# Performance work log

Measured on AMD Instinct MI355X. Metric: run time of the kernel, lower is better.

Reference implementation:

```python
import jax, jax.numpy as jnp
import numpy as np
from jax import lax

B, S, T, E, H, V = 32, 64, 48, 512, 1024, 32000
PAD = 0


def lstm_cell(x, h, c, W_ih, W_hh, b_ih, b_hh):
    # PyTorch gate order: i, f, g, o
    gates = x @ W_ih.T + b_ih + h @ W_hh.T + b_hh
    i, f, g, o = jnp.split(gates, 4, axis=-1)
    c = jax.nn.sigmoid(f) * c + jax.nn.sigmoid(i) * jnp.tanh(g)
    h = jax.nn.sigmoid(o) * jnp.tanh(c)
    return h, c


def setup_inputs() -> dict:
    key = jax.random.key(0)
    ks = jax.random.split(key, 24)
    sc = 0.02
    n = lambda k, shape: jax.random.normal(k, shape, jnp.float32) * sc
    src_emb = n(ks[0], (V, E)).at[PAD].set(0.0)
    tgt_emb = n(ks[1], (V, E)).at[PAD].set(0.0)
    inp = {
        "input_sequences": jax.random.randint(ks[2], (B, S), 0, V),
        "target_sequences": jax.random.randint(ks[3], (B, T), 0, V),
        "src_emb": src_emb,
        "tgt_emb": tgt_emb,
        "enc_Wih_f": n(ks[4], (4 * H, E)),
        "enc_Whh_f": n(ks[5], (4 * H, H)),
        "enc_bih_f": n(ks[6], (4 * H,)),
        "enc_bhh_f": n(ks[7], (4 * H,)),
        "enc_Wih_b": n(ks[8], (4 * H, E)),
        "enc_Whh_b": n(ks[9], (4 * H, H)),
        "enc_bih_b": n(ks[10], (4 * H,)),
        "enc_bhh_b": n(ks[11], (4 * H,)),
        "dec_Wih": n(ks[12], (4 * H, E + H)),
        "dec_Whh": n(ks[13], (4 * H, H)),
        "dec_bih": n(ks[14], (4 * H,)),
        "dec_bhh": n(ks[15], (4 * H,)),
        "W_init_h": n(ks[16], (H, 2 * H)),
        "W_init_c": n(ks[17], (H, 2 * H)),
        "W_att": n(ks[18], (H, 2 * H)),
        "W_comb": n(ks[19], (H, 3 * H)),
        "W_proj": n(ks[20], (V, H)),
    }
    return inp


def reference(input_sequences, target_sequences, src_emb, tgt_emb,
              enc_Wih_f, enc_Whh_f, enc_bih_f, enc_bhh_f,
              enc_Wih_b, enc_Whh_b, enc_bih_b, enc_bhh_b,
              dec_Wih, dec_Whh, dec_bih, dec_bhh,
              W_init_h, W_init_c, W_att, W_comb, W_proj):
    bsz = input_sequences.shape[0]
    x_src = src_emb[input_sequences.T]  # (S, B, E) time-major

    def make_enc_step(W_ih, W_hh, b_ih, b_hh):
        def step(carry, x):
            h, c = carry
            h, c = lstm_cell(x, h, c, W_ih, W_hh, b_ih, b_hh)
            return (h, c), h
        return step

    h0 = jnp.zeros((bsz, H), x_src.dtype)
    c0 = jnp.zeros((bsz, H), x_src.dtype)
    # bidirectional encoder
    (hf, cf), hs_f = lax.scan(make_enc_step(enc_Wih_f, enc_Whh_f, enc_bih_f, enc_bhh_f), (h0, c0), x_src)
    (hb, cb), hs_b = lax.scan(make_enc_step(enc_Wih_b, enc_Whh_b, enc_bih_b, enc_bhh_b), (h0, c0), x_src[::-1])
    enc_h = jnp.concatenate([hs_f, hs_b[::-1]], axis=-1).transpose(1, 0, 2)  # (B, S, 2H)
    last_hidden = jnp.concatenate([hf, hb], axis=-1)  # (B, 2H)
    last_cell = jnp.concatenate([cf, cb], axis=-1)

    dec_h0 = last_hidden @ W_init_h.T
    dec_c0 = last_cell @ W_init_c.T
    enc_att = enc_h @ W_att.T  # (B, S, H)

    x_tgt = tgt_emb[target_sequences.T]  # (T, B, E)

    def dec_step(carry, e_t):
        h, c, prev_out = carry
        x = jnp.concatenate([e_t, prev_out], axis=-1)  # (B, E+H)
        h, c = lstm_cell(x, h, c, dec_Wih, dec_Whh, dec_bih, dec_bhh)
        scores = jnp.einsum('bh,bsh->bs', h, enc_att)
        attn = jax.nn.softmax(scores, axis=-1)
        ctx = jnp.einsum('bs,bsd->bd', attn, enc_h)  # (B, 2H)
        out = jnp.concatenate([h, ctx], axis=-1) @ W_comb.T  # (B, H)
        return (h, c, out), out

    prev0 = jnp.zeros((bsz, H), x_src.dtype)
    _, outs = lax.scan(dec_step, (dec_h0, dec_c0, prev0), x_tgt)  # (T, B, H)

    logits = outs @ W_proj.T  # (T, B, V)
    P = jax.nn.log_softmax(logits, axis=-1)
    tgt = target_sequences.T  # (T, B)
    # P[t] predicts tgt[t+1]; torch.gather with smaller index truncates P to T-1 steps
    gold = jnp.take_along_axis(P[:-1], tgt[1:][..., None], axis=-1)[..., 0]  # (T-1, B)
    scores = gold.sum(axis=0)  # (B,)
    return scores
```

## Files before the change

### kernel.cpp

```cpp
#include <hip/hip_runtime.h>

typedef short v8s __attribute__((ext_vector_type(8)));
typedef float v4f __attribute__((ext_vector_type(4)));
typedef unsigned short u16;

#define DI __device__ __forceinline__
#define MFMA(a, b, c) __builtin_amdgcn_mfma_f32_16x16x32_bf16(a, b, c, 0, 0, 0)

constexpr int B = 32, S = 64, T = 48, E = 512, H = 1024, V = 32000;
constexpr int TP = T - 1;
constexpr int MROWS = TP * B;
constexpr int NCH = 250;

DI u16 f2bf(float f) {
    unsigned u = __float_as_uint(f);
    unsigned r = (u + 0x7FFFu + ((u >> 16) & 1u)) >> 16;
    return (u16)r;
}
DI float bf2f(u16 h) { return __uint_as_float(((unsigned)h) << 16); }
DI v8s load8(const u16* p) { return *reinterpret_cast<const v8s*>(p); }

typedef __attribute__((address_space(1))) const unsigned int gu32;
typedef __attribute__((address_space(3))) unsigned int lu32;
DI void gload_lds16(const u16* g, u16* l) {
    __builtin_amdgcn_global_load_lds((gu32*)g, (lu32*)l, 16, 0, 0);
}

DI void cstore(unsigned* p, unsigned v) {
    __hip_atomic_store(p, v, __ATOMIC_RELAXED, __HIP_MEMORY_SCOPE_AGENT);
}
DI int cload(const int* p) {
    return __hip_atomic_load(p, __ATOMIC_RELAXED, __HIP_MEMORY_SCOPE_AGENT);
}

DI void gbar2(int* bar, int bid, int nblk, int v) {
    __syncthreads();
    if (bid == 0) {
        int t = threadIdx.x;
        if (t > 0 && t < nblk) {
            while (cload(bar + 16 + t * 4) < v) __builtin_amdgcn_s_sleep(1);
        }
        __syncthreads();
        if (t == 0)
            __hip_atomic_store(bar, v, __ATOMIC_RELAXED, __HIP_MEMORY_SCOPE_AGENT);
    } else {
        if (threadIdx.x == 0) {
            __hip_atomic_store(bar + 16 + bid * 4, v, __ATOMIC_RELAXED,
                               __HIP_MEMORY_SCOPE_AGENT);
            while (cload(bar) < v) __builtin_amdgcn_s_sleep(2);
        }
        __syncthreads();
    }
}

__global__ __launch_bounds__(256) void k_cvt(const float* __restrict__ s,
                                             u16* __restrict__ d, int n4) {
    int i = blockIdx.x * 256 + threadIdx.x;
    if (i >= n4) return;
    float4 v = reinterpret_cast<const float4*>(s)[i];
    ushort4 o;
    o.x = f2bf(v.x); o.y = f2bf(v.y); o.z = f2bf(v.z); o.w = f2bf(v.w);
    reinterpret_cast<ushort4*>(d)[i] = o;
}

struct CvtD {
    const float* src[11];
    u16* dst[11];
    int n4[11];
    int start[12];
};
__global__ __launch_bounds__(256) void k_cvtm(CvtD d) {
    int blk = blockIdx.x;
    int seg = 0;
    #pragma unroll
    for (int q = 0; q < 11; ++q)
        if (blk >= d.start[q + 1]) seg = q + 1;
    int i = (blk - d.start[seg]) * 256 + threadIdx.x;
    if (i >= d.n4[seg]) return;
    float4 v = reinterpret_cast<const float4*>(d.src[seg])[i];
    ushort4 o;
    o.x = f2bf(v.x); o.y = f2bf(v.y); o.z = f2bf(v.z); o.w = f2bf(v.w);
    reinterpret_cast<ushort4*>(d.dst[seg])[i] = o;
}

__global__ __launch_bounds__(256) void k_embed(const int* __restrict__ seq, int seqstr,
                                               int nsteps, const float* __restrict__ emb,
                                               u16* __restrict__ out) {
    int i = blockIdx.x * 256 + threadIdx.x;
    int total = nsteps * B * (E / 4);
    if (i >= total) return;
    int q = i & 127;
    int sb = i >> 7;
    int b = sb & 31;
    int s = sb >> 5;
    int tok = seq[b * seqstr + s];
    float4 v = reinterpret_cast<const float4*>(emb + (size_t)tok * E)[q];
    ushort4 o;
    o.x = f2bf(v.x); o.y = f2bf(v.y); o.z = f2bf(v.z); o.w = f2bf(v.w);
    reinterpret_cast<ushort4*>(out + ((size_t)(s * B + b)) * E)[q] = o;
}

__global__ __launch_bounds__(256) void k_ench(const u16* __restrict__ hsf,
                                              const u16* __restrict__ hsb,
                                              u16* __restrict__ ench) {
    int id = blockIdx.x * 256 + threadIdx.x;
    int d8 = id & 255; int s = (id >> 8) & 63; int b = id >> 14;
    int d0 = d8 * 8;
    const u16* src = (d0 < H) ? hsf + (((size_t)(s + 1) * B + b)) * H + d0
                              : hsb + (((size_t)(S - s) * B + b)) * H + (d0 - H);
    *reinterpret_cast<v8s*>(ench + ((size_t)b * S + s) * 2 * H + d0) = load8(src);
}

__global__ __launch_bounds__(256) void k_transp(const u16* __restrict__ in,
                                                u16* __restrict__ out, int K, int N) {
    __shared__ u16 t[64][72];
    int nt = blockIdx.x * 64, kt = blockIdx.y * 64;
    int tid = threadIdx.x;
    int r = tid >> 2, cq = (tid & 3) * 16;
    v8s v0 = load8(in + (size_t)(kt + r) * N + nt + cq);
    v8s v1 = load8(in + (size_t)(kt + r) * N + nt + cq + 8);
    #pragma unroll
    for (int e = 0; e < 8; ++e) { t[r][cq + e] = (u16)v0[e]; t[r][cq + 8 + e] = (u16)v1[e]; }
    __syncthreads();
    v8s o0, o1;
    #pragma unroll
    for (int e = 0; e < 8; ++e) { o0[e] = (short)t[cq + e][r]; o1[e] = (short)t[cq + 8 + e][r]; }
    *reinterpret_cast<v8s*>(out + (size_t)(nt + r) * K + kt + cq) = o0;
    *reinterpret_cast<v8s*>(out + (size_t)(nt + r) * K + kt + cq + 8) = o1;
}

__global__ __launch_bounds__(256) void k_tile(const u16* __restrict__ A, int astr,
                                              const u16* __restrict__ W, int wstr,
                                              float* __restrict__ outf,
                                              u16* __restrict__ outb, int ostr,
                                              int ktiles) {
    __shared__ __align__(16) u16 As[128 * 64];
    __shared__ __align__(16) u16 Bs[128 * 64];
    const int tid = threadIdx.x;
    const int lane = tid & 63, wv = tid >> 6;
    const int l15 = lane & 15, lg = lane >> 4;
    const int wr = wv >> 1, wc = wv & 1;
    const int m0 = blockIdx.y * 128, n0 = blockIdx.x * 128;
    const int srow = lane >> 3, sc_ = lane & 7;

    v4f acc[4][4];
    #pragma unroll
    for (int i = 0; i < 4; ++i)
        #pragma unroll
        for (int j = 0; j < 4; ++j) acc[i][j] = v4f{0.f, 0.f, 0.f, 0.f};

    for (int kt = 0; kt < ktiles; ++kt) {
        const int kb = kt * 64;
        #pragma unroll
        for (int i = 0; i < 4; ++i) {
            int chunk = wv * 4 + i;
            int row = chunk * 8 + srow;
            int csw = (sc_ ^ (row & 7)) << 3;
            gload_lds16(A + (size_t)(m0 + row) * astr + kb + csw, As + chunk * 512);
            gload_lds16(W + (size_t)(n0 + row) * wstr + kb + csw, Bs + chunk * 512);
        }
        __syncthreads();
        #pragma unroll
        for (int kk = 0; kk < 2; ++kk) {
            int sw = (((kk << 2) | lg) ^ (l15 & 7)) << 3;
            v8s af[4], bfv[4];
            #pragma unroll
            for (int mi = 0; mi < 4; ++mi)
                af[mi] = load8(As + (wr * 64 + mi * 16 + l15) * 64 + sw);
            #pragma unroll
            for (int ni = 0; ni < 4; ++ni)
                bfv[ni] = load8(Bs + (wc * 64 + ni * 16 + l15) * 64 + sw);
            #pragma unroll
            for (int mi = 0; mi < 4; ++mi)
                #pragma unroll
                for (int ni = 0; ni < 4; ++ni)
                    acc[mi][ni] = MFMA(af[mi], bfv[ni], acc[mi][ni]);
        }
        __syncthreads();
    }
    #pragma unroll
    for (int mi = 0; mi < 4; ++mi)
        #pragma unroll
        for (int rr = 0; rr < 4; ++rr) {
            int row = m0 + wr * 64 + mi * 16 + lg * 4 + rr;
            #pragma unroll
            for (int ni = 0; ni < 4; ++ni) {
                int col = n0 + wc * 64 + ni * 16 + l15;
                if (outf) outf[(size_t)row * ostr + col] = acc[mi][ni][rr];
                else      outb[(size_t)row * ostr + col] = f2bf(acc[mi][ni][rr]);
            }
        }
}

struct Seg { const u16* a; int astr; const u16* w; int wstr; int k; };

__global__ __launch_bounds__(512) void k_mm(Seg s1, Seg s2, float* __restrict__ outf,
                                            u16* __restrict__ outb, int ostr, int ks,
                                            int sub) {
    const int tid = threadIdx.x;
    const int wv = tid >> 6, lane = tid & 63;
    const int l15 = lane & 15, lg = lane >> 4;
    const int wrow = blockIdx.x * 16 + l15;
    const int k0 = wv * ks, k1 = k0 + ks;
    v4f acc0 = {0.f, 0.f, 0.f, 0.f}, acc1 = {0.f, 0.f, 0.f, 0.f};
    int base = 0;
    auto doseg = [&](const Seg& sg) {
        if (sg.k == 0) return;
        int s0 = k0 > base ? k0 : base;
        int send = base + sg.k;
        int s1e = k1 < send ? k1 : send;
        const u16* wp = sg.w + (size_t)wrow * sg.wstr + 8 * lg;
        const u16* a0p = sg.a + (size_t)l15 * sg.astr + 8 * lg;
        const u16* a1p = sg.a + (size_t)(16 + l15) * sg.astr + 8 * lg;
        #pragma unroll 2
        for (int k = s0; k < s1e; k += 32) {
            int kl = k - base;
            v8s bf = load8(wp + kl);
            v8s af0 = load8(a0p + kl);
            v8s af1 = load8(a1p + kl);
            acc0 = MFMA(af0, bf, acc0);
            acc1 = MFMA(af1, bf, acc1);
        }
        base += sg.k;
    };
    doseg(s1); doseg(s2);

    __shared__ float g[8][32][16];
    #pragma unroll
    for (int r = 0; r < 4; ++r) {
        g[wv][lg * 4 + r][l15] = acc0[r];
        g[wv][16 + lg * 4 + r][l15] = acc1[r];
    }
    __syncthreads();
    {
        int b = tid >> 4, cl = tid & 15;
        float v = 0.f;
        #pragma unroll
        for (int w = 0; w < 8; ++w) v += g[w][b][cl];
        int col = blockIdx.x * 16 + cl;
        size_t idx = (size_t)b * ostr + col;
        if (outb)      outb[idx] = f2bf(v);
        else if (sub)  outf[idx] -= v;
        else           outf[idx] = v;
    }
}

__global__ __launch_bounds__(512) void k_enc(
    const float* __restrict__ xgF, const float* __restrict__ xgB,
    const u16* __restrict__ whhf, const u16* __restrict__ whhb,
    const float* __restrict__ bihF, const float* __restrict__ bhhF,
    const float* __restrict__ bihB, const float* __restrict__ bhhB,
    u16* __restrict__ hsf, u16* __restrict__ hsb,
    float* __restrict__ cfinal, int* __restrict__ bars) {
    const int blk = blockIdx.x;
    const int dir = blk >> 8, bid = blk & 255;
    const int tid = threadIdx.x;
    const u16* whh = dir ? whhb : whhf;
    const float* xg = dir ? xgB : xgF;
    const float* bih = dir ? bihB : bihF;
    const float* bhh = dir ? bhhB : bhhF;
    u16* hs = dir ? hsb : hsf;
    int* bar = bars + dir * 2048;
    const int j0 = bid * 4;
    __shared__ u16 wlds[16 * 1024];
    __shared__ float glds[8][32][16];
    __shared__ u16 htmp[32][4];
    {
        int r = tid >> 5, kc = tid & 31;
        int gate = r >> 2, jl = r & 3;
        const u16* src = whh + (size_t)(gate * H + j0 + jl) * H;
        #pragma unroll
        for (int i = 0; i < 4; ++i) {
            int c = kc + 32 * i;
            v8s v = load8(src + c * 8);
            *reinterpret_cast<v8s*>(wlds + r * 1024 + ((c ^ (r & 7)) * 8)) = v;
        }
    }
    float creg = 0.f;
    const int pb = tid >> 2, pj = tid & 3;
    float bsum[4];
    if (tid < 128) {
        #pragma unroll
        for (int gt = 0; gt < 4; ++gt)
            bsum[gt] = bih[gt * H + j0 + pj] + bhh[gt * H + j0 + pj];
    }
    __syncthreads();
    const int wv = tid >> 6, lane = tid & 63, l15 = lane & 15, lg = lane >> 4;
    for (int s = 0; s < S; ++s) {
        float xv[4];
        if (tid < 128) {
            int xrow = ((dir ? (S - 1 - s) : s) * 32 + pb) * 4096;
            const float* xr = xg + xrow + j0 + pj;
            #pragma unroll
            for (int gt = 0; gt < 4; ++gt) xv[gt] = xr[gt * H];
        }
        const u16* hp = hs + (size_t)s * (B * H);
        const u16* a0 = hp + (size_t)l15 * H + wv * 128 + 8 * lg;
        const u16* a1 = a0 + (size_t)16 * H;
        v4f acc0 = {0.f, 0.f, 0.f, 0.f}, acc1 = {0.f, 0.f, 0.f, 0.f};
        #pragma unroll
        for (int kb = 0; kb < 4; ++kb) {
            int c = wv * 16 + kb * 4 + lg;
            v8s bf = load8(wlds + l15 * 1024 + ((c ^ (l15 & 7)) * 8));
            v8s af0 = load8(a0 + kb * 32);
            v8s af1 = load8(a1 + kb * 32);
            acc0 = MFMA(af0, bf, acc0);
            acc1 = MFMA(af1, bf, acc1);
        }
        #pragma unroll
        for (int r = 0; r < 4; ++r) {
            glds[wv][lg * 4 + r][l15] = acc0[r];
            glds[wv][16 + lg * 4 + r][l15] = acc1[r];
        }
        __syncthreads();
        if (tid < 128) {
            float gv[4];
            #pragma unroll
            for (int gt = 0; gt < 4; ++gt) {
                float v = 0.f;
                #pragma unroll
                for (int w = 0; w < 8; ++w) v += glds[w][pb][gt * 4 + pj];
                gv[gt] = v + xv[gt] + bsum[gt];
            }
            float si = 1.f / (1.f + expf(-gv[0]));
            float sf = 1.f / (1.f + expf(-gv[1]));
            float tg = tanhf(gv[2]);
            float so = 1.f / (1.f + expf(-gv[3]));
            creg = sf * creg + si * tg;
            htmp[pb][pj] = f2bf(so * tanhf(creg));
        }
        __syncthreads();
        if (tid < 64) {
            int rb = tid >> 1, c2 = (tid & 1) * 2;
            unsigned val = (unsigned)htmp[rb][c2] | ((unsigned)htmp[rb][c2 + 1] << 16);
            cstore((unsigned*)(hs + (size_t)(s + 1) * (B * H) + (size_t)rb * H + j0 + c2), val);
        }
        if (s < S - 1) gbar2(bar, bid, 256, s + 1);
    }
    if (tid < 128) cfinal[(size_t)dir * B * H + (size_t)pb * H + j0 + pj] = creg;
}

__global__ __launch_bounds__(512) void k_dec(
    const float* __restrict__ xgD, const u16* __restrict__ dwhh,
    const u16* __restrict__ wfuse, const float* __restrict__ bih,
    const float* __restrict__ bhh, const float* __restrict__ decc,
    const u16* __restrict__ encab, const u16* __restrict__ ench,
    u16* __restrict__ hc, int* __restrict__ bar) {
    const int bid = blockIdx.x, tid = threadIdx.x;
    const int j0 = bid * 4;
    __shared__ u16 wlds[16 * 3072];
    __shared__ float glds[8][32][16];
    __shared__ float hl[1056];
    __shared__ float sc[64], aw[64];
    __shared__ float cpart[4][128][2];
    __shared__ u16 htmp[32][4];
    {
        int r = tid >> 5, kc = tid & 31;
        int gate = r >> 2, jl = r & 3;
        int grow = gate * H + j0 + jl;
        for (int i = 0; i < 12; ++i) {
            int c = kc + 32 * i;
            int k = c * 8;
            v8s wf = load8(wfuse + (size_t)grow * 3072 + k);
            if (k < 1024) {
                v8s wh = load8(dwhh + (size_t)grow * 1024 + k);
                #pragma unroll
                for (int e = 0; e < 8; ++e)
                    wf[e] = (short)f2bf(bf2f((u16)wf[e]) + bf2f((u16)wh[e]));
            }
            *reinterpret_cast<v8s*>(wlds + r * 3072 + ((c ^ (r & 7)) * 8)) = wf;
        }
    }
    const int pb = tid >> 2, pj = tid & 3;
    float creg = 0.f;
    float bsum[4];
    if (tid < 128) {
        creg = decc[(size_t)pb * H + j0 + pj];
        #pragma unroll
        for (int gt = 0; gt < 4; ++gt)
            bsum[gt] = bih[gt * H + j0 + pj] + bhh[gt * H + j0 + pj];
    }
    __syncthreads();
    const int wv = tid >> 6, lane = tid & 63, l15 = lane & 15, lg = lane >> 4;
    const int ab = bid >> 3, ach = bid & 7;
    for (int t = 0; t < T; ++t) {
        const u16* hp = hc + (size_t)t * (B * 3072);
        u16* hn = hc + (size_t)(t + 1) * (B * 3072);
        float xv[4];
        if (tid < 128) {
            const float* xr = xgD + (size_t)(t * 32 + pb) * 4096 + j0 + pj;
            #pragma unroll
            for (int gt = 0; gt < 4; ++gt) xv[gt] = xr[gt * H];
        }
        const u16* a0 = hp + (size_t)l15 * 3072 + wv * 384 + 8 * lg;
        const u16* a1 = a0 + (size_t)16 * 3072;
        v4f acc0 = {0.f, 0.f, 0.f, 0.f}, acc1 = {0.f, 0.f, 0.f, 0.f};
        #pragma unroll
        for (int kb = 0; kb < 12; ++kb) {
            int c = wv * 48 + kb * 4 + lg;
            v8s bf = load8(wlds + l15 * 3072 + ((c ^ (l15 & 7)) * 8));
            v8s af0 = load8(a0 + kb * 32);
            v8s af1 = load8(a1 + kb * 32);
            acc0 = MFMA(af0, bf, acc0);
            acc1 = MFMA(af1, bf, acc1);
        }
        #pragma unroll
        for (int r = 0; r < 4; ++r) {
            glds[wv][lg * 4 + r][l15] = acc0[r];
            glds[wv][16 + lg * 4 + r][l15] = acc1[r];
        }
        __syncthreads();
        if (tid < 128) {
            float gv[4];
            #pragma unroll
            for (int gt = 0; gt < 4; ++gt) {
                float v = 0.f;
                #pragma unroll
                for (int w = 0; w < 8; ++w) v += glds[w][pb][gt * 4 + pj];
                gv[gt] = v + xv[gt] + bsum[gt];
            }
            float si = 1.f / (1.f + expf(-gv[0]));
            float sf = 1.f / (1.f + expf(-gv[1]));
            float tg = tanhf(gv[2]);
            float so = 1.f / (1.f + expf(-gv[3]));
            creg = sf * creg + si * tg;
            htmp[pb][pj] = f2bf(so * tanhf(creg));
        }
        __syncthreads();
        if (tid < 64) {
            int rb = tid >> 1, c2 = (tid & 1) * 2;
            unsigned val = (unsigned)htmp[rb][c2] | ((unsigned)htmp[rb][c2 + 1] << 16);
            cstore((unsigned*)(hn + (size_t)rb * 3072 + j0 + c2), val);
        }
        gbar2(bar, bid, 256, 2 * t + 1);
        {
            const u16* hb = hn + (size_t)ab * 3072;
            for (int i = tid; i < 1024; i += 512)
                hl[((i >> 7) * 132) + (i & 127)] = bf2f(hb[i]);
            __syncthreads();
            {
                int si2 = tid >> 3, pt = tid & 7;
                const u16* ap = encab + ((size_t)(ab * 64 + si2)) * 1024 + pt * 128;
                const float* hq = hl + pt * 132;
                float ps = 0.f;
                #pragma unroll
                for (int x = 0; x < 16; ++x) {
                    v8s v = load8(ap + x * 8);
                    #pragma unroll
                    for (int e = 0; e < 8; ++e) ps += bf2f((u16)v[e]) * hq[x * 8 + e];
                }
                ps += __shfl_xor(ps, 1); ps += __shfl_xor(ps, 2); ps += __shfl_xor(ps, 4);
                if (pt == 0) sc[si2] = ps;
            }
            __syncthreads();
            if (tid < 64) {
                float v = sc[tid];
                float m = v;
                #pragma unroll
                for (int o = 32; o; o >>= 1) m = fmaxf(m, __shfl_xor(m, o));
                float e = expf(v - m), sum = e;
                #pragma unroll
                for (int o = 32; o; o >>= 1) sum += __shfl_xor(sum, o);
                aw[tid] = e / sum;
            }
            __syncthreads();
            {
                int q = tid >> 7, dp = tid & 127;
                int d = ach * 256 + dp * 2;
                const u16* ep = ench + (size_t)ab * S * 2048 + (size_t)(q * 16) * 2048 + d;
                float c0 = 0.f, c1 = 0.f;
                #pragma unroll 8
                for (int s2 = 0; s2 < 16; ++s2) {
                    unsigned uv = *reinterpret_cast<const unsigned*>(ep);
                    float w = aw[q * 16 + s2];
                    c0 += w * bf2f((u16)(uv & 0xFFFF));
                    c1 += w * bf2f((u16)(uv >> 16));
                    ep += 2048;
                }
                cpart[q][dp][0] = c0;
                cpart[q][dp][1] = c1;
            }
            __syncthreads();
            if (tid < 128) {
                float c0 = cpart[0][tid][0] + cpart[1][tid][0]
                         + cpart[2][tid][0] + cpart[3][tid][0];
                float c1 = cpart[0][tid][1] + cpart[1][tid][1]
                         + cpart[2][tid][1] + cpart[3][tid][1];
                unsigned ov = ((unsigned)f2bf(c1) << 16) | f2bf(c0);
                cstore((unsigned*)(hn + (size_t)ab * 3072 + 1024 + ach * 256 + tid * 2), ov);
            }
        }
        if (t < T - 1) gbar2(bar, bid, 256, 2 * t + 2);
    }
}

__global__ __launch_bounds__(512) void k_proj(const u16* __restrict__ A,
                                              const u16* __restrict__ W,
                                              const int* __restrict__ tgt,
                                              float* __restrict__ pmax,
                                              float* __restrict__ psum,
                                              float* __restrict__ pgold) {
    __shared__ __align__(16) u16 As[256 * 64];
    __shared__ __align__(16) u16 Bs[128 * 64];
    __shared__ float red[256][2][3];
    const int tid = threadIdx.x;
    const int lane = tid & 63, wv = tid >> 6;
    const int l15 = lane & 15, lg = lane >> 4;
    const int wr = wv >> 1, wc = wv & 1;
    int orig = blockIdx.x;
    int xcd = orig & 7, loc = orig >> 3;
    int wgid = (xcd < 4 ? xcd * 188 : 752 + (xcd - 4) * 187) + loc;
    int nt = wgid / 6, mt = wgid % 6;
    const int m0 = mt * 256, n0 = nt * 128;
    const int srow = lane >> 3, sc_ = lane & 7;

    v4f acc[4][4];
    #pragma unroll
    for (int i = 0; i < 4; ++i)
        #pragma unroll
        for (int j = 0; j < 4; ++j) acc[i][j] = v4f{0.f, 0.f, 0.f, 0.f};

    for (int kt = 0; kt < 16; ++kt) {
        const int kb = kt * 64;
        #pragma unroll
        for (int i = 0; i < 4; ++i) {
            int chunk = wv * 4 + i;
            int row = chunk * 8 + srow;
            int csw = (sc_ ^ (row & 7)) << 3;
            gload_lds16(A + (size_t)(m0 + row) * 1024 + kb + csw, As + chunk * 512);
        }
        #pragma unroll
        for (int i = 0; i < 2; ++i) {
            int chunk = wv * 2 + i;
            int row = chunk * 8 + srow;
            int csw = (sc_ ^ (row & 7)) << 3;
            gload_lds16(W + (size_t)(n0 + row) * 1024 + kb + csw, Bs + chunk * 512);
        }
        __syncthreads();
        #pragma unroll
        for (int kk = 0; kk < 2; ++kk) {
            int sw = (((kk << 2) | lg) ^ (l15 & 7)) << 3;
            v8s af[4], bfv[4];
            #pragma unroll
            for (int mi = 0; mi < 4; ++mi)
                af[mi] = load8(As + (wr * 64 + mi * 16 + l15) * 64 + sw);
            #pragma unroll
            for (int ni = 0; ni < 4; ++ni)
                bfv[ni] = load8(Bs + (wc * 64 + ni * 16 + l15) * 64 + sw);
            #pragma unroll
            for (int mi = 0; mi < 4; ++mi)
                #pragma unroll
                for (int ni = 0; ni < 4; ++ni)
                    acc[mi][ni] = MFMA(af[mi], bfv[ni], acc[mi][ni]);
        }
        __syncthreads();
    }
    #pragma unroll
    for (int mi = 0; mi < 4; ++mi) {
        #pragma unroll
        for (int rr = 0; rr < 4; ++rr) {
            int lrow = wr * 64 + mi * 16 + lg * 4 + rr;
            int grow = m0 + lrow;
            float vmax = -1e30f;
            #pragma unroll
            for (int ni = 0; ni < 4; ++ni) vmax = fmaxf(vmax, acc[mi][ni][rr]);
            #pragma unroll
            for (int x = 1; x < 16; x <<= 1) vmax = fmaxf(vmax, __shfl_xor(vmax, x));
            float se = 0.f;
            #pragma unroll
            for (int ni = 0; ni < 4; ++ni) se += expf(acc[mi][ni][rr] - vmax);
            #pragma unroll
            for (int x = 1; x < 16; x <<= 1) se += __shfl_xor(se, x);
            int t = grow >> 5, b = grow & 31;
            int g = (grow < MROWS) ? tgt[b * T + t + 1] : -1;
            float gv = 0.f;
            #pragma unroll
            for (int ni = 0; ni < 4; ++ni) {
                int col = n0 + wc * 64 + ni * 16 + l15;
                if (col == g) gv = acc[mi][ni][rr];
            }
            #pragma unroll
            for (int x = 1; x < 16; x <<= 1) gv += __shfl_xor(gv, x);
            if (l15 == 0) {
                red[lrow][wc][0] = vmax;
                red[lrow][wc][1] = se;
                red[lrow][wc][2] = gv;
            }
        }
    }
    __syncthreads();
    if (tid < 256) {
        int grow = m0 + tid;
        if (grow < MROWS) {
            float ma = red[tid][0][0], mb = red[tid][1][0];
            float M = fmaxf(ma, mb);
            float Sv = red[tid][0][1] * expf(ma - M) + red[tid][1][1] * expf(mb - M);
            float G = red[tid][0][2] + red[tid][1][2];
            size_t idx = (size_t)grow * NCH + nt;
            pmax[idx] = M; psum[idx] = Sv; pgold[idx] = G;
        }
    }
}

__global__ __launch_bounds__(256) void k_lse(const float* __restrict__ pmax,
                                             const float* __restrict__ psum,
                                             const float* __restrict__ pgold,
                                             float* __restrict__ logP) {
    int item = blockIdx.x * 4 + (threadIdx.x >> 6);
    int lane = threadIdx.x & 63;
    if (item >= MROWS) return;
    float m = -1e30f, g = 0.f;
    for (int c = lane; c < NCH; c += 64) {
        size_t idx = (size_t)item * NCH + c;
        m = fmaxf(m, pmax[idx]);
        g += pgold[idx];
    }
    for (int o = 32; o; o >>= 1) m = fmaxf(m, __shfl_xor(m, o));
    float s = 0.f;
    for (int c = lane; c < NCH; c += 64) {
        size_t idx = (size_t)item * NCH + c;
        s += psum[idx] * expf(pmax[idx] - m);
    }
    for (int o = 32; o; o >>= 1) { s += __shfl_xor(s, o); g += __shfl_xor(g, o); }
    if (lane == 0) logP[item] = g - (m + logf(s));
}

__global__ __launch_bounds__(64) void k_final(const float* __restrict__ logP,
                                              float* __restrict__ out) {
    int b = threadIdx.x;
    if (b < 32) {
        float s = 0.f;
        for (int t = 0; t < TP; ++t) s += logP[t * 32 + b];
        out[b] = s;
    }
}

extern "C" void kernel_launch(void* const* d_in, const int* in_sizes, int n_in,
                              void* d_out, int out_size, void* d_ws, size_t ws_size,
                              hipStream_t stream) {
    const int*   seq_in  = (const int*)d_in[0];
    const int*   seq_tgt = (const int*)d_in[1];
    const float* src_emb = (const float*)d_in[2];
    const float* tgt_emb = (const float*)d_in[3];
    const float* eWihF = (const float*)d_in[4];
    const float* eWhhF = (const float*)d_in[5];
    const float* eBihF = (const float*)d_in[6];
    const float* eBhhF = (const float*)d_in[7];
    const float* eWihB = (const float*)d_in[8];
    const float* eWhhB = (const float*)d_in[9];
    const float* eBihB = (const float*)d_in[10];
    const float* eBhhB = (const float*)d_in[11];
    const float* dWih  = (const float*)d_in[12];
    const float* dWhh  = (const float*)d_in[13];
    const float* dBih  = (const float*)d_in[14];
    const float* dBhh  = (const float*)d_in[15];
    const float* WinH  = (const float*)d_in[16];
    const float* WinC  = (const float*)d_in[17];
    const float* Watt  = (const float*)d_in[18];
    const float* Wcomb = (const float*)d_in[19];
    const float* Wproj = (const float*)d_in[20];

    char* ws = (char*)d_ws;
    size_t off = 0;
    auto alloc = [&](size_t bytes) -> char* {
        off = (off + 255) & ~(size_t)255;
        char* p = ws + off;
        off += bytes;
        return p;
    };
    const size_t G4 = 4 * (size_t)H;
    const size_t slot = (size_t)B * H;
    u16* wihf = (u16*)alloc(G4 * E * 2);
    u16* whhf = (u16*)alloc(G4 * H * 2);
    u16* wihb = (u16*)alloc(G4 * E * 2);
    u16* whhb = (u16*)alloc(G4 * H * 2);
    u16* dwih = (u16*)alloc(G4 * (E + H) * 2);
    u16* dwhh = (u16*)alloc(G4 * H * 2);
    u16* winh = (u16*)alloc((size_t)H * 2 * H * 2);
    u16* winc = (u16*)alloc((size_t)H * 2 * H * 2);
    u16* watt = (u16*)alloc((size_t)H * 2 * H * 2);
    u16* wcmb = (u16*)alloc((size_t)H * 3 * H * 2);
    u16* wprj = (u16*)alloc((size_t)V * H * 2);
    u16* wcmbT = (u16*)alloc((size_t)3 * H * H * 2);
    u16* wfuse = (u16*)alloc((size_t)G4 * 3 * H * 2);
    u16* xsrc  = (u16*)alloc((size_t)S * B * E * 2);
    u16* xtgt  = (u16*)alloc((size_t)T * B * E * 2);
    u16* hsf   = (u16*)alloc((size_t)(S + 1) * slot * 2);
    u16* hsb   = (u16*)alloc((size_t)(S + 1) * slot * 2);
    u16* ench  = (u16*)alloc((size_t)B * S * 2 * H * 2);
    u16* encab = (u16*)alloc((size_t)B * S * H * 2);
    u16* hc    = (u16*)alloc((size_t)(T + 1) * B * 3072 * 2);
    u16* outsb = (u16*)alloc((size_t)(T * B) * H * 2);
    u16* lcbf  = (u16*)alloc(2 * slot * 2);
    float* xgF  = (float*)alloc((size_t)S * B * G4 * 4);
    float* xgB  = (float*)alloc((size_t)S * B * G4 * 4);
    float* xgD  = (float*)alloc((size_t)T * B * G4 * 4);
    float* cf2  = (float*)alloc(2 * slot * 4);
    float* decc = (float*)alloc(slot * 4);
    float* pmax  = (float*)alloc((size_t)MROWS * NCH * 4);
    float* psum  = (float*)alloc((size_t)MROWS * NCH * 4);
    float* pgold = (float*)alloc((size_t)MROWS * NCH * 4);
    float* logP  = (float*)alloc((size_t)MROWS * 4);
    int* bars = (int*)alloc(3 * 2048 * 4);
    (void)ws_size; (void)in_sizes; (void)n_in; (void)out_size;

    hipMemsetAsync(hsf, 0, slot * 2, stream);
    hipMemsetAsync(hsb, 0, slot * 2, stream);
    hipMemsetAsync(hc, 0, (size_t)B * 3072 * 2, stream);
    hipMemsetAsync(bars, 0, 3 * 2048 * 4, stream);

    {
        CvtD d;
        const float* srcs[11] = {eWihF, eWhhF, eWihB, eWhhB, dWih, dWhh,
                                 WinH, WinC, Watt, Wcomb, Wproj};
        u16* dsts[11] = {wihf, whhf, wihb, whhb, dwih, dwhh,
                         winh, winc, watt, wcmb, wprj};
        size_t ns[11] = {G4 * E, G4 * H, G4 * E, G4 * H, G4 * (E + H), G4 * H,
                         (size_t)H * 2 * H, (size_t)H * 2 * H, (size_t)H * 2 * H,
                         (size_t)H * 3 * H, (size_t)V * H};
        int blk = 0;
        for (int i = 0; i < 11; ++i) {
            d.src[i] = srcs[i];
            d.dst[i] = dsts[i];
            d.n4[i] = (int)(ns[i] / 4);
            d.start[i] = blk;
            blk += (d.n4[i] + 255) / 256;
        }
        d.start[11] = blk;
        k_cvtm<<<dim3(blk), dim3(256), 0, stream>>>(d);
    }

    k_embed<<<dim3((S * B * (E / 4) + 255) / 256), dim3(256), 0, stream>>>(
        seq_in, S, S, src_emb, xsrc);
    k_embed<<<dim3((T * B * (E / 4) + 255) / 256), dim3(256), 0, stream>>>(
        seq_tgt, T, T, tgt_emb, xtgt);

    k_transp<<<dim3(3 * H / 64, H / 64), dim3(256), 0, stream>>>(wcmb, wcmbT, H, 3 * H);

    k_tile<<<dim3(32, 16), dim3(256), 0, stream>>>(xsrc, E, wihf, E, xgF, nullptr, 4096, 8);
    k_tile<<<dim3(32, 16), dim3(256), 0, stream>>>(xsrc, E, wihb, E, xgB, nullptr, 4096, 8);
    k_tile<<<dim3(32, 12), dim3(256), 0, stream>>>(xtgt, E, dwih, E + H, xgD, nullptr, 4096, 8);
    k_tile<<<dim3(24, 32), dim3(256), 0, stream>>>(dwih + E, E + H, wcmbT, H,
                                                   nullptr, wfuse, 3 * H, 16);

    k_enc<<<dim3(512), dim3(512), 0, stream>>>(xgF, xgB, whhf, whhb,
                                               eBihF, eBhhF, eBihB, eBhhB,
                                               hsf, hsb, cf2, bars);

    k_ench<<<dim3(B * S * (2 * H / 8) / 256), dim3(256), 0, stream>>>(hsf, hsb, ench);
    k_tile<<<dim3(8, 16), dim3(256), 0, stream>>>(ench, 2 * H, watt, 2 * H,
                                                  nullptr, encab, H, 32);
    {
        int n4 = (int)(2 * slot / 4);
        k_cvt<<<dim3((n4 + 255) / 256), dim3(256), 0, stream>>>(cf2, lcbf, n4);
    }

    {
        Seg a1{hsf + (size_t)S * slot, H, winh, 2 * H, H};
        Seg a2{hsb + (size_t)S * slot, H, winh + H, 2 * H, H};
        k_mm<<<dim3(H / 16), dim3(512), 0, stream>>>(a1, a2, nullptr, hc, 3072,
                                                     2 * H / 8, 0);
        Seg c1{lcbf, H, winc, 2 * H, H};
        Seg c2{lcbf + slot, H, winc + H, 2 * H, H};
        k_mm<<<dim3(H / 16), dim3(512), 0, stream>>>(c1, c2, decc, nullptr, H,
                                                     2 * H / 8, 0);
        Seg f1{hc, 3072, wfuse, 3 * H, H};
        Seg f0{nullptr, 0, nullptr, 0, 0};
        k_mm<<<dim3(G4 / 16), dim3(512), 0, stream>>>(f1, f0, xgD, nullptr, 4096,
                                                      H / 8, 1);
    }

    k_dec<<<dim3(256), dim3(512), 0, stream>>>(xgD, dwhh, wfuse, dBih, dBhh, decc,
                                               encab, ench, hc, bars + 4096);

    k_tile<<<dim3(8, 12), dim3(256), 0, stream>>>(hc + B * 3072, 3 * H, wcmb, 3 * H,
                                                  nullptr, outsb, H, 48);

    k_proj<<<dim3(1500), dim3(512), 0, stream>>>(outsb, wprj, seq_tgt, pmax, psum, pgold);
    k_lse<<<dim3((MROWS + 3) / 4), dim3(256), 0, stream>>>(pmax, psum, pgold, logP);
    k_final<<<dim3(1), dim3(64), 0, stream>>>(logP, (float*)d_out);
}
```

Baseline: 1.420 ms.

## Halve encoder block count and batch four input GEMMs into one launch

The recurrent encoder kernel now gives each block 8 hidden units instead of 4, so it runs 128 blocks per direction with a 32-row weight slab in LDS and twice the MFMAs per wave. The goal is cheaper grid-wide barrier synchronisation on every timestep. Separately, the four independent input-projection GEMMs go into a single segmented tile kernel launch, removing launch gaps and letting their tiles share the GPU. The cost is fewer CUs active per encoder step and higher LDS use per block.

New measurement: 1.385 ms (median of 2 runs). 1.03x faster.

```diff
diff --git a/kernel.cpp b/kernel.cpp
--- a/kernel.cpp
+++ b/kernel.cpp
@@ -141,6 +141,84 @@
     const int l15 = lane & 15, lg = lane >> 4;
     const int wr = wv >> 1, wc = wv & 1;
     const int m0 = blockIdx.y * 128, n0 = blockIdx.x * 128;
+    const int srow = lane >> 3, sc_ = lane & 7;
+
+    v4f acc[4][4];
+    #pragma unroll
+    for (int i = 0; i < 4; ++i)
+        #pragma unroll
+        for (int j = 0; j < 4; ++j) acc[i][j] = v4f{0.f, 0.f, 0.f, 0.f};
+
+    for (int kt = 0; kt < ktiles; ++kt) {
+        const int kb = kt * 64;
+        #pragma unroll
+        for (int i = 0; i < 4; ++i) {
+            int chunk = wv * 4 + i;
+            int row = chunk * 8 + srow;
+            int csw = (sc_ ^ (row & 7)) << 3;
+            gload_lds16(A + (size_t)(m0 + row) * astr + kb + csw, As + chunk * 512);
+            gload_lds16(W + (size_t)(n0 + row) * wstr + kb + csw, Bs + chunk * 512);
+        }
+        __syncthreads();
+        #pragma unroll
+        for (int kk = 0; kk < 2; ++kk) {
+            int sw = (((kk << 2) | lg) ^ (l15 & 7)) << 3;
+            v8s af[4], bfv[4];
+            #pragma unroll
+            for (int mi = 0; mi < 4; ++mi)
+                af[mi] = load8(As + (wr * 64 + mi * 16 + l15) * 64 + sw);
+            #pragma unroll
+            for (int ni = 0; ni < 4; ++ni)
+                bfv[ni] = load8(Bs + (wc * 64 + ni * 16 + l15) * 64 + sw);
+            #pragma unroll
+            for (int mi = 0; mi < 4; ++mi)
+                #pragma unroll
+                for (int ni = 0; ni < 4; ++ni)
+                    acc[mi][ni] = MFMA(af[mi], bfv[ni], acc[mi][ni]);
+        }
+        __syncthreads();
+    }
+    #pragma unroll
+    for (int mi = 0; mi < 4; ++mi)
+        #pragma unroll
+        for (int rr = 0; rr < 4; ++rr) {
+            int row = m0 + wr * 64 + mi * 16 + lg * 4 + rr;
+            #pragma unroll
+            for (int ni = 0; ni < 4; ++ni) {
+                int col = n0 + wc * 64 + ni * 16 + l15;
+                if (outf) outf[(size_t)row * ostr + col] = acc[mi][ni][rr];
+                else      outb[(size_t)row * ostr + col] = f2bf(acc[mi][ni][rr]);
+            }
+        }
+}
+
+struct T4 {
+    const u16* A[4]; int astr[4];
+    const u16* W[4]; int wstr[4];
+    float* outf[4]; u16* outb[4]; int ostr[4];
+    int kt[4]; int nx[4]; int start[5];
+};
+__global__ __launch_bounds__(256) void k_tile4(T4 p) {
+    __shared__ __align__(16) u16 As[128 * 64];
+    __shared__ __align__(16) u16 Bs[128 * 64];
+    int blk = blockIdx.x;
+    int seg = 0;
+    #pragma unroll
+    for (int q = 0; q < 3; ++q)
+        if (blk >= p.start[q + 1]) seg = q + 1;
+    int lid = blk - p.start[seg];
+    const int n0 = (lid % p.nx[seg]) * 128;
+    const int m0 = (lid / p.nx[seg]) * 128;
+    const u16* A = p.A[seg];
+    const u16* W = p.W[seg];
+    const int astr = p.astr[seg], wstr = p.wstr[seg], ostr = p.ostr[seg];
+    float* outf = p.outf[seg];
+    u16* outb = p.outb[seg];
+    const int ktiles = p.kt[seg];
+    const int tid = threadIdx.x;
+    const int lane = tid & 63, wv = tid >> 6;
+    const int l15 = lane & 15, lg = lane >> 4;
+    const int wr = wv >> 1, wc = wv & 1;
     const int srow = lane >> 3, sc_ = lane & 7;
 
     v4f acc[4][4];
@@ -253,7 +331,7 @@
     u16* __restrict__ hsf, u16* __restrict__ hsb,
     float* __restrict__ cfinal, int* __restrict__ bars) {
     const int blk = blockIdx.x;
-    const int dir = blk >> 8, bid = blk & 255;
+    const int dir = blk >> 7, bid = blk & 127;
     const int tid = threadIdx.x;
     const u16* whh = dir ? whhb : whhf;
     const float* xg = dir ? xgB : xgF;
@@ -261,25 +339,25 @@
     const float* bhh = dir ? bhhB : bhhF;
     u16* hs = dir ? hsb : hsf;
     int* bar = bars + dir * 2048;
-    const int j0 = bid * 4;
-    __shared__ u16 wlds[16 * 1024];
-    __shared__ float glds[8][32][16];
-    __shared__ u16 htmp[32][4];
+    const int j0 = bid * 8;
+    __shared__ u16 wlds[32 * 1024];
+    __shared__ float glds[8][32][34];
+    __shared__ u16 htmp[32][8];
     {
-        int r = tid >> 5, kc = tid & 31;
-        int gate = r >> 2, jl = r & 3;
+        int r = tid >> 4, kc = tid & 15;
+        int gate = r >> 3, jl = r & 7;
         const u16* src = whh + (size_t)(gate * H + j0 + jl) * H;
         #pragma unroll
-        for (int i = 0; i < 4; ++i) {
-            int c = kc + 32 * i;
+        for (int i = 0; i < 8; ++i) {
+            int c = kc + 16 * i;
             v8s v = load8(src + c * 8);
             *reinterpret_cast<v8s*>(wlds + r * 1024 + ((c ^ (r & 7)) * 8)) = v;
         }
     }
     float creg = 0.f;
-    const int pb = tid >> 2, pj = tid & 3;
+    const int pb = tid >> 3, pj = tid & 7;
     float bsum[4];
-    if (tid < 128) {
+    if (tid < 256) {
         #pragma unroll
         for (int gt = 0; gt < 4; ++gt)
             bsum[gt] = bih[gt * H + j0 + pj] + bhh[gt * H + j0 + pj];
@@ -288,7 +366,7 @@
     const int wv = tid >> 6, lane = tid & 63, l15 = lane & 15, lg = lane >> 4;
     for (int s = 0; s < S; ++s) {
         float xv[4];
-        if (tid < 128) {
+        if (tid < 256) {
             int xrow = ((dir ? (S - 1 - s) : s) * 32 + pb) * 4096;
             const float* xr = xg + xrow + j0 + pj;
             #pragma unroll
@@ -297,29 +375,36 @@
         const u16* hp = hs + (size_t)s * (B * H);
         const u16* a0 = hp + (size_t)l15 * H + wv * 128 + 8 * lg;
         const u16* a1 = a0 + (size_t)16 * H;
-        v4f acc0 = {0.f, 0.f, 0.f, 0.f}, acc1 = {0.f, 0.f, 0.f, 0.f};
+        v4f acc00 = {0,0,0,0}, acc01 = {0,0,0,0}, acc10 = {0,0,0,0}, acc11 = {0,0,0,0};
         #pragma unroll
         for (int kb = 0; kb < 4; ++kb) {
             int c = wv * 16 + kb * 4 + lg;
-            v8s bf = load8(wlds + l15 * 1024 + ((c ^ (l15 & 7)) * 8));
+            int w0 = l15;
+            int w1 = 16 + l15;
+            v8s bf0 = load8(wlds + w0 * 1024 + ((c ^ (w0 & 7)) * 8));
+            v8s bf1 = load8(wlds + w1 * 1024 + ((c ^ (w1 & 7)) * 8));
             v8s af0 = load8(a0 + kb * 32);
             v8s af1 = load8(a1 + kb * 32);
-            acc0 = MFMA(af0, bf, acc0);
-            acc1 = MFMA(af1, bf, acc1);
+            acc00 = MFMA(af0, bf0, acc00);
+            acc10 = MFMA(af0, bf1, acc10);
+            acc01 = MFMA(af1, bf0, acc01);
+            acc11 = MFMA(af1, bf1, acc11);
         }
         #pragma unroll
         for (int r = 0; r < 4; ++r) {
-            glds[wv][lg * 4 + r][l15] = acc0[r];
-            glds[wv][16 + lg * 4 + r][l15] = acc1[r];
-        }
-        __syncthreads();
-        if (tid < 128) {
+            glds[wv][lg * 4 + r][l15] = acc00[r];
+            glds[wv][lg * 4 + r][16 + l15] = acc10[r];
+            glds[wv][16 + lg * 4 + r][l15] = acc01[r];
+            glds[wv][16 + lg * 4 + r][16 + l15] = acc11[r];
+        }
+        __syncthreads();
+        if (tid < 256) {
             float gv[4];
             #pragma unroll
             for (int gt = 0; gt < 4; ++gt) {
                 float v = 0.f;
                 #pragma unroll
-                for (int w = 0; w < 8; ++w) v += glds[w][pb][gt * 4 + pj];
+                for (int w = 0; w < 8; ++w) v += glds[w][pb][gt * 8 + pj];
                 gv[gt] = v + xv[gt] + bsum[gt];
             }
             float si = 1.f / (1.f + expf(-gv[0]));
@@ -330,14 +415,14 @@
             htmp[pb][pj] = f2bf(so * tanhf(creg));
         }
         __syncthreads();
-        if (tid < 64) {
-            int rb = tid >> 1, c2 = (tid & 1) * 2;
+        if (tid < 128) {
+            int rb = tid >> 2, c2 = (tid & 3) * 2;
             unsigned val = (unsigned)htmp[rb][c2] | ((unsigned)htmp[rb][c2 + 1] << 16);
             cstore((unsigned*)(hs + (size_t)(s + 1) * (B * H) + (size_t)rb * H + j0 + c2), val);
         }
-        if (s < S - 1) gbar2(bar, bid, 256, s + 1);
-    }
-    if (tid < 128) cfinal[(size_t)dir * B * H + (size_t)pb * H + j0 + pj] = creg;
+        if (s < S - 1) gbar2(bar, bid, 128, s + 1);
+    }
+    if (tid < 256) cfinal[(size_t)dir * B * H + (size_t)pb * H + j0 + pj] = creg;
 }
 
 __global__ __launch_bounds__(512) void k_dec(
@@ -737,13 +822,25 @@
 
     k_transp<<<dim3(3 * H / 64, H / 64), dim3(256), 0, stream>>>(wcmb, wcmbT, H, 3 * H);
 
-    k_tile<<<dim3(32, 16), dim3(256), 0, stream>>>(xsrc, E, wihf, E, xgF, nullptr, 4096, 8);
-    k_tile<<<dim3(32, 16), dim3(256), 0, stream>>>(xsrc, E, wihb, E, xgB, nullptr, 4096, 8);
-    k_tile<<<dim3(32, 12), dim3(256), 0, stream>>>(xtgt, E, dwih, E + H, xgD, nullptr, 4096, 8);
-    k_tile<<<dim3(24, 32), dim3(256), 0, stream>>>(dwih + E, E + H, wcmbT, H,
-                                                   nullptr, wfuse, 3 * H, 16);
-
-    k_enc<<<dim3(512), dim3(512), 0, stream>>>(xgF, xgB, whhf, whhb,
+    {
+        T4 p;
+        p.A[0] = xsrc; p.astr[0] = E; p.W[0] = wihf; p.wstr[0] = E;
+        p.outf[0] = xgF; p.outb[0] = nullptr; p.ostr[0] = 4096; p.kt[0] = 8; p.nx[0] = 32;
+        p.A[1] = xsrc; p.astr[1] = E; p.W[1] = wihb; p.wstr[1] = E;
+        p.outf[1] = xgB; p.outb[1] = nullptr; p.ostr[1] = 4096; p.kt[1] = 8; p.nx[1] = 32;
+        p.A[2] = xtgt; p.astr[2] = E; p.W[2] = dwih; p.wstr[2] = E + H;
+        p.outf[2] = xgD; p.outb[2] = nullptr; p.ostr[2] = 4096; p.kt[2] = 8; p.nx[2] = 32;
+        p.A[3] = dwih + E; p.astr[3] = E + H; p.W[3] = wcmbT; p.wstr[3] = H;
+        p.outf[3] = nullptr; p.outb[3] = wfuse; p.ostr[3] = 3 * H; p.kt[3] = 16; p.nx[3] = 24;
+        p.start[0] = 0;
+        p.start[1] = 512;
+        p.start[2] = 1024;
+        p.start[3] = 1408;
+        p.start[4] = 1408 + 768;
+        k_tile4<<<dim3(p.start[4]), dim3(256), 0, stream>>>(p);
+    }
+
+    k_enc<<<dim3(256), dim3(512), 0, stream>>>(xgF, xgB, whhf, whhb,
                                                eBihF, eBhhF, eBihB, eBhhB,
                                                hsf, hsb, cf2, bars);
 
```
